# Performance work log

Hardware: AMD Instinct MI355X
Metric: run time of the kernel (lower is better)

## Reference

```python
import jax, jax.numpy as jnp
import numpy as np

NU = 100000  # num 'user' nodes
NI = 100000  # num 'item' nodes
E = 600000   # edges per relation
IN_DIM = 128
HID = 128
OUT = 64


def setup_inputs() -> dict:
    key = jax.random.key(0)
    ks = jax.random.split(key, 14)
    return {
        "x_user": jax.random.normal(ks[0], (NU, IN_DIM), jnp.float32),
        "x_item": jax.random.normal(ks[1], (NI, IN_DIM), jnp.float32),
        "W_proj": jax.random.normal(ks[2], (IN_DIM, HID), jnp.float32) / np.sqrt(IN_DIM),
        "b_proj": jax.random.normal(ks[3], (HID,), jnp.float32) * 0.01,
        "W_out": jax.random.normal(ks[4], (HID, OUT), jnp.float32) / np.sqrt(HID),
        "b_out": jax.random.normal(ks[5], (OUT,), jnp.float32) * 0.01,
        "al1": jax.random.normal(ks[6], (1,), jnp.float32),
        "ar1": jax.random.normal(ks[7], (1,), jnp.float32),
        "al2": jax.random.normal(ks[8], (1,), jnp.float32),
        "ar2": jax.random.normal(ks[9], (1,), jnp.float32),
        "e1_src": jax.random.randint(ks[10], (E,), 0, NU, jnp.int32),  # user->user
        "e1_dst": jax.random.randint(ks[11], (E,), 0, NU, jnp.int32),
        "e2_src": jax.random.randint(ks[12], (E,), 0, NI, jnp.int32),  # item->user
        "e2_dst": jax.random.randint(ks[13], (E,), 0, NU, jnp.int32),
    }


def reference(x_user, x_item, W_proj, b_proj, W_out, b_out,
              al1, ar1, al2, ar2, e1_src, e1_dst, e2_src, e2_dst):
    # Shared projection for every node type
    h_user = x_user @ W_proj + b_proj  # [NU, HID]
    h_item = x_item @ W_proj + b_proj  # [NI, HID]

    # Relation ('user','u2u','user'): msg = h_src*al + h_dst*ar, scatter-add to dst
    msg1 = h_user[e1_src] * al1 + h_user[e1_dst] * ar1  # [E, HID]
    out_user = jax.ops.segment_sum(msg1, e1_dst, num_segments=NU)

    # Relation ('item','i2u','user')
    msg2 = h_item[e2_src] * al2 + h_user[e2_dst] * ar2  # [E, HID]
    out_user = out_user + jax.ops.segment_sum(msg2, e2_dst, num_segments=NU)

    # 'item' receives no messages -> zeros
    out_item = jnp.zeros_like(h_item)

    out_user = jax.nn.elu(out_user)
    out_item = jax.nn.elu(out_item)

    # out_layer applied only to 'user'
    out_user = out_user @ W_out + b_out  # [NU, OUT]
    return out_user, out_item
```

## Files before the change

### kernel.cpp

```cpp
#include <hip/hip_runtime.h>
#include <hip/hip_bf16.h>
#include <math.h>

#define NUSER 100000
#define NITEM 100000
#define NEDGE 600000
#define HID   128
#define OUTD  64
#define LDA   136
#define LDF   132
#define PROJ_BLOCKS ((NUSER + NITEM) / 64)
#define EPB   ((2 * NEDGE + PROJ_BLOCKS - 1) / PROJ_BLOCKS)

typedef __attribute__((ext_vector_type(8))) short  bf16x8;
typedef __attribute__((ext_vector_type(4))) float  f32x4;
typedef __attribute__((ext_vector_type(4))) unsigned short u16x4;

__device__ inline unsigned short f2bf(float f) {
    __hip_bfloat16 h = __float2bfloat16(f);
    return *reinterpret_cast<unsigned short*>(&h);
}

__device__ inline void bf2x(unsigned int u, float& lo, float& hi) {
    union { unsigned int i; float f; } a, b;
    a.i = u << 16;
    b.i = u & 0xffff0000u;
    lo = a.f; hi = b.f;
}

__global__ void prep(const float* __restrict__ W, unsigned short* __restrict__ wt,
                     int* __restrict__ deg) {
    int i = blockIdx.x * 256 + threadIdx.x;
    if (i < 2 * NUSER) deg[i] = 0;
    if (i < 128 * 128) {
        int k = i >> 7, c = i & 127;
        wt[c * 128 + k] = f2bf(W[i]);
    }
}

__global__ void count_rank(const int* __restrict__ e1d, const int* __restrict__ e2d,
                           int* __restrict__ deg1, int* __restrict__ deg2,
                           int* __restrict__ rank) {
    int i = blockIdx.x * blockDim.x + threadIdx.x;
    if (i < NEDGE)            rank[i] = atomicAdd(&deg1[e1d[i]], 1);
    else if (i < 2 * NEDGE)   rank[i] = atomicAdd(&deg2[e2d[i - NEDGE]], 1);
}

#define SCAN_BLOCKS 391

__global__ __launch_bounds__(256) void scanA(
    const int* __restrict__ deg1, const int* __restrict__ deg2,
    int* __restrict__ off, int* __restrict__ bsum)
{
    __shared__ int sh[256];
    int t = threadIdx.x;
    int i = blockIdx.x * 256 + t;
    int d = (i < NUSER) ? deg1[i] + deg2[i] : 0;
    sh[t] = d;
    __syncthreads();
    for (int dd = 1; dd < 256; dd <<= 1) {
        int v = (t >= dd) ? sh[t - dd] : 0;
        __syncthreads();
        sh[t] += v;
        __syncthreads();
    }
    if (i < NUSER) off[i] = (t > 0) ? sh[t - 1] : 0;
    if (t == 255) bsum[blockIdx.x] = sh[255];
}

__global__ __launch_bounds__(512) void scanB(int* __restrict__ bsum, int* __restrict__ off) {
    __shared__ int sh[512];
    int t = threadIdx.x;
    int v = (t < SCAN_BLOCKS) ? bsum[t] : 0;
    sh[t] = v;
    __syncthreads();
    for (int dd = 1; dd < 512; dd <<= 1) {
        int x = (t >= dd) ? sh[t - dd] : 0;
        __syncthreads();
        sh[t] += x;
        __syncthreads();
    }
    if (t < SCAN_BLOCKS) bsum[t] = (t > 0) ? sh[t - 1] : 0;
    if (t == 511) off[NUSER] = sh[511];
}

__global__ __launch_bounds__(256) void scanC(int* __restrict__ off, const int* __restrict__ bsum) {
    int i = blockIdx.x * 256 + threadIdx.x;
    if (i < NUSER) off[i] += bsum[blockIdx.x];
}

__global__ __launch_bounds__(256) void proj_fill(
    const float* __restrict__ xu, const float* __restrict__ xi,
    const unsigned short* __restrict__ wt, const float* __restrict__ b,
    unsigned short* __restrict__ h,
    const int* __restrict__ e1s, const int* __restrict__ e1d,
    const int* __restrict__ e2s, const int* __restrict__ e2d,
    const int* __restrict__ off, const int* __restrict__ deg1,
    const int* __restrict__ rank, int* __restrict__ adj)
{
    __shared__ unsigned short Al[64 * LDA];
    const int tid = threadIdx.x;
    const int r0  = blockIdx.x * 64;

    float4 v[8];
    #pragma unroll
    for (int j = 0; j < 8; j++) {
        int i = tid + j * 256;
        int row = i >> 5, c4 = i & 31;
        int gr = r0 + row;
        const float4* src = (gr < NUSER)
            ? (const float4*)(xu + (size_t)gr * 128)
            : (const float4*)(xi + (size_t)(gr - NUSER) * 128);
        v[j] = src[c4];
    }
    #pragma unroll
    for (int j = 0; j < 8; j++) {
        int i = tid + j * 256;
        int row = i >> 5, c4 = i & 31;
        u16x4 p;
        p.x = f2bf(v[j].x); p.y = f2bf(v[j].y); p.z = f2bf(v[j].z); p.w = f2bf(v[j].w);
        *(u16x4*)&Al[row * LDA + c4 * 4] = p;
    }
    __syncthreads();

    const int w    = tid >> 6;
    const int lane = tid & 63;
    const int lrow = lane & 15;
    const int lk   = (lane >> 4) * 8;

    bf16x8 bfrag[4][2];
    #pragma unroll
    for (int kc = 0; kc < 4; kc++) {
        const int ko = kc * 32 + lk;
        bfrag[kc][0] = *(const bf16x8*)&wt[(size_t)(w * 32 + lrow) * 128 + ko];
        bfrag[kc][1] = *(const bf16x8*)&wt[(size_t)(w * 32 + 16 + lrow) * 128 + ko];
    }

    f32x4 acc[4][2] = {};
    #pragma unroll
    for (int kc = 0; kc < 4; kc++) {
        const int ko = kc * 32 + lk;
        #pragma unroll
        for (int rt = 0; rt < 4; rt++) {
            bf16x8 aa = *(const bf16x8*)&Al[(rt * 16 + lrow) * LDA + ko];
            acc[rt][0] = __builtin_amdgcn_mfma_f32_16x16x32_bf16(aa, bfrag[kc][0], acc[rt][0], 0, 0, 0);
            acc[rt][1] = __builtin_amdgcn_mfma_f32_16x16x32_bf16(aa, bfrag[kc][1], acc[rt][1], 0, 0, 0);
        }
    }

    __syncthreads();
    const float bv0 = b[w * 32 + lrow];
    const float bv1 = b[w * 32 + 16 + lrow];
    #pragma unroll
    for (int rt = 0; rt < 4; rt++) {
        #pragma unroll
        for (int ct = 0; ct < 2; ct++) {
            int col = w * 32 + ct * 16 + lrow;
            float bv = ct ? bv1 : bv0;
            #pragma unroll
            for (int r = 0; r < 4; r++) {
                int row = rt * 16 + (lane >> 4) * 4 + r;
                Al[row * LDA + col] = f2bf(acc[rt][ct][r] + bv);
            }
        }
    }
    __syncthreads();

    for (int i = tid; i < 1024; i += 256) {
        int row = i >> 4, c8 = i & 15;
        *(bf16x8*)&h[(size_t)(r0 + row) * 128 + c8 * 8] =
            *(const bf16x8*)&Al[row * LDA + c8 * 8];
    }

    const int base = blockIdx.x * EPB;
    const int lim  = (base + EPB < 2 * NEDGE) ? base + EPB : 2 * NEDGE;
    for (int i = base + tid; i < lim; i += 256) {
        int src, dst, slot;
        if (i < NEDGE) {
            src  = e1s[i];
            dst  = e1d[i];
            slot = off[dst] + rank[i];
        } else {
            int j = i - NEDGE;
            src  = NUSER + e2s[j];
            dst  = e2d[j];
            slot = off[dst] + deg1[dst] + rank[i];
        }
        adj[slot] = src;
    }
}

__global__ __launch_bounds__(256) void gather(
    const unsigned short* __restrict__ h, const int* __restrict__ adj,
    const int* __restrict__ off, const int* __restrict__ deg1,
    const int* __restrict__ deg2,
    const float* __restrict__ al1p, const float* __restrict__ ar1p,
    const float* __restrict__ al2p, const float* __restrict__ ar2p,
    unsigned int* __restrict__ accb)
{
    int wid  = (int)((blockIdx.x * 256 + threadIdx.x) >> 6);
    int lane = threadIdx.x & 63;
    if (wid >= NUSER) return;

    const unsigned int* h32 = (const unsigned int*)h;

    const float al1 = al1p[0], al2 = al2p[0];
    const float sc  = ar1p[0] * (float)deg1[wid] + ar2p[0] * (float)deg2[wid];

    float lo, hi;
    bf2x(h32[(size_t)wid * 64 + lane], lo, hi);
    float sx = sc * lo, sy = sc * hi;

    int e    = off[wid];
    int eend = off[wid + 1];

    for (; e + 8 <= eend; e += 8) {
        int s[8];
        #pragma unroll
        for (int j = 0; j < 8; j++) s[j] = adj[e + j];
        unsigned int u[8];
        #pragma unroll
        for (int j = 0; j < 8; j++) u[j] = h32[(size_t)s[j] * 64 + lane];
        #pragma unroll
        for (int j = 0; j < 8; j++) {
            float a = (s[j] < NUSER) ? al1 : al2;
            float x, y; bf2x(u[j], x, y);
            sx = fmaf(a, x, sx); sy = fmaf(a, y, sy);
        }
    }
    if (e + 4 <= eend) {
        int s[4];
        #pragma unroll
        for (int j = 0; j < 4; j++) s[j] = adj[e + j];
        unsigned int u[4];
        #pragma unroll
        for (int j = 0; j < 4; j++) u[j] = h32[(size_t)s[j] * 64 + lane];
        #pragma unroll
        for (int j = 0; j < 4; j++) {
            float a = (s[j] < NUSER) ? al1 : al2;
            float x, y; bf2x(u[j], x, y);
            sx = fmaf(a, x, sx); sy = fmaf(a, y, sy);
        }
        e += 4;
    }
    for (; e < eend; e++) {
        int s0 = adj[e];
        float a0 = (s0 < NUSER) ? al1 : al2;
        float x0, y0;
        bf2x(h32[(size_t)s0 * 64 + lane], x0, y0);
        sx = fmaf(a0, x0, sx); sy = fmaf(a0, y0, sy);
    }

    sx = sx > 0.f ? sx : expm1f(sx);
    sy = sy > 0.f ? sy : expm1f(sy);
    unsigned int pk = ((unsigned int)f2bf(sy) << 16) | (unsigned int)f2bf(sx);
    accb[(size_t)wid * 64 + lane] = pk;
}

__global__ __launch_bounds__(256) void finalize(
    const unsigned int* __restrict__ accb, const float* __restrict__ Wo,
    const float* __restrict__ bo, float* __restrict__ out)
{
    __shared__ float Wl[128 * 64];
    __shared__ float Al[64 * LDF];
    const int tid = threadIdx.x;
    const int n0  = blockIdx.x * 64;

    for (int i = tid; i < 128 * 64 / 4; i += 256)
        ((float4*)Wl)[i] = ((const float4*)Wo)[i];

    for (int i = tid; i < 4096; i += 256) {
        int row = i >> 6, d = i & 63;
        int gr = n0 + row;
        float lo = 0.f, hi = 0.f;
        if (gr < NUSER) bf2x(accb[(size_t)gr * 64 + d], lo, hi);
        *(float2*)&Al[row * LDF + d * 2] = make_float2(lo, hi);
    }
    __syncthreads();

    const int tr = tid >> 4;
    const int tc = tid & 15;

    float s[4][4];
    {
        float4 bv = *(const float4*)&bo[tc * 4];
        #pragma unroll
        for (int i = 0; i < 4; i++) {
            s[i][0] = bv.x; s[i][1] = bv.y; s[i][2] = bv.z; s[i][3] = bv.w;
        }
    }

    for (int k0 = 0; k0 < 128; k0 += 4) {
        float4 av[4];
        #pragma unroll
        for (int i = 0; i < 4; i++)
            av[i] = *(const float4*)&Al[(tr * 4 + i) * LDF + k0];
        #pragma unroll
        for (int kk = 0; kk < 4; kk++) {
            float4 wv = *(const float4*)&Wl[(k0 + kk) * 64 + tc * 4];
            #pragma unroll
            for (int i = 0; i < 4; i++) {
                float a = (&av[i].x)[kk];
                s[i][0] = fmaf(a, wv.x, s[i][0]);
                s[i][1] = fmaf(a, wv.y, s[i][1]);
                s[i][2] = fmaf(a, wv.z, s[i][2]);
                s[i][3] = fmaf(a, wv.w, s[i][3]);
            }
        }
    }

    #pragma unroll
    for (int i = 0; i < 4; i++) {
        int gr = n0 + tr * 4 + i;
        if (gr < NUSER) {
            float4 o = make_float4(s[i][0], s[i][1], s[i][2], s[i][3]);
            *(float4*)&out[(size_t)gr * 64 + tc * 4] = o;
        }
    }
}

extern "C" void kernel_launch(void* const* d_in, const int* in_sizes, int n_in,
                              void* d_out, int out_size, void* d_ws, size_t ws_size,
                              hipStream_t stream) {
    const float* xu  = (const float*)d_in[0];
    const float* xi  = (const float*)d_in[1];
    const float* Wp  = (const float*)d_in[2];
    const float* bp  = (const float*)d_in[3];
    const float* Wo  = (const float*)d_in[4];
    const float* bo  = (const float*)d_in[5];
    const float* al1 = (const float*)d_in[6];
    const float* ar1 = (const float*)d_in[7];
    const float* al2 = (const float*)d_in[8];
    const float* ar2 = (const float*)d_in[9];
    const int* e1s = (const int*)d_in[10];
    const int* e1d = (const int*)d_in[11];
    const int* e2s = (const int*)d_in[12];
    const int* e2d = (const int*)d_in[13];

    float* out   = (float*)d_out;
    float* oitem = out + (size_t)NUSER * OUTD;

    unsigned short* h    = (unsigned short*)d_ws;
    unsigned short* wt   = h + (size_t)(NUSER + NITEM) * HID;
    unsigned int*   accb = (unsigned int*)(wt + 128 * 128);

    int* meta = (int*)out;
    int* deg1 = meta;
    int* deg2 = meta + NUSER;
    int* off  = meta + 2 * NUSER;
    int* bsum = meta + 3 * NUSER + 64;
    int* adj  = meta + 3 * NUSER + 1024;
    int* rank = adj + 2 * NEDGE;

    hipMemsetAsync(oitem, 0, (size_t)NITEM * HID * sizeof(float), stream);

    prep<<<(2 * NUSER + 255) / 256, 256, 0, stream>>>(Wp, wt, deg1);

    count_rank<<<(2 * NEDGE + 255) / 256, 256, 0, stream>>>(e1d, e2d, deg1, deg2, rank);

    scanA<<<SCAN_BLOCKS, 256, 0, stream>>>(deg1, deg2, off, bsum);
    scanB<<<1, 512, 0, stream>>>(bsum, off);
    scanC<<<SCAN_BLOCKS, 256, 0, stream>>>(off, bsum);

    proj_fill<<<PROJ_BLOCKS, 256, 0, stream>>>(xu, xi, wt, bp, h,
                                               e1s, e1d, e2s, e2d,
                                               off, deg1, rank, adj);

    gather<<<(NUSER * 64) / 256, 256, 0, stream>>>(h, adj, off, deg1, deg2,
                                                   al1, ar1, al2, ar2, accb);

    finalize<<<(NUSER + 63) / 64, 256, 0, stream>>>(accb, Wo, bo, out);
}
```

Measured before the change: 227.4 us.

## Process two nodes per wave in gather and enlarge projection tiles

The gather kernel now gives each wavefront two destination nodes and interleaves their neighbor loads, so more independent memory requests are in flight per wave. The projection kernel moves from 64-row to 128-row tiles, staged in two halves, with a clamped item index, bounds-checked stores and a fixed three-iteration edge-fill loop. count_rank handles two edges per thread. Together these aim to hide gather latency and cut launch and block overhead, at the cost of higher register pressure, fewer waves in flight, and imbalance when the paired nodes have different degrees.

```diff
diff --git a/kernel.cpp b/kernel.cpp
--- a/kernel.cpp
+++ b/kernel.cpp
@@ -9,7 +9,8 @@
 #define OUTD  64
 #define LDA   136
 #define LDF   132
-#define PROJ_BLOCKS ((NUSER + NITEM) / 64)
+#define BLKR  128
+#define PROJ_BLOCKS ((NUSER + NITEM + BLKR - 1) / BLKR)
 #define EPB   ((2 * NEDGE + PROJ_BLOCKS - 1) / PROJ_BLOCKS)
 
 typedef __attribute__((ext_vector_type(8))) short  bf16x8;
@@ -38,12 +39,18 @@
     }
 }
 
+__device__ inline void cr_one(int i, const int* e1d, const int* e2d,
+                              int* deg1, int* deg2, int* rank) {
+    if (i < NEDGE)            rank[i] = atomicAdd(&deg1[e1d[i]], 1);
+    else if (i < 2 * NEDGE)   rank[i] = atomicAdd(&deg2[e2d[i - NEDGE]], 1);
+}
+
 __global__ void count_rank(const int* __restrict__ e1d, const int* __restrict__ e2d,
                            int* __restrict__ deg1, int* __restrict__ deg2,
                            int* __restrict__ rank) {
-    int i = blockIdx.x * blockDim.x + threadIdx.x;
-    if (i < NEDGE)            rank[i] = atomicAdd(&deg1[e1d[i]], 1);
-    else if (i < 2 * NEDGE)   rank[i] = atomicAdd(&deg2[e2d[i - NEDGE]], 1);
+    int i0 = blockIdx.x * 512 + threadIdx.x;
+    cr_one(i0, e1d, e2d, deg1, deg2, rank);
+    cr_one(i0 + 256, e1d, e2d, deg1, deg2, rank);
 }
 
 #define SCAN_BLOCKS 391
@@ -98,28 +105,36 @@
     const int* __restrict__ off, const int* __restrict__ deg1,
     const int* __restrict__ rank, int* __restrict__ adj)
 {
-    __shared__ unsigned short Al[64 * LDA];
+    __shared__ unsigned short Al[BLKR * LDA];
     const int tid = threadIdx.x;
-    const int r0  = blockIdx.x * 64;
-
-    float4 v[8];
-    #pragma unroll
-    for (int j = 0; j < 8; j++) {
-        int i = tid + j * 256;
-        int row = i >> 5, c4 = i & 31;
-        int gr = r0 + row;
-        const float4* src = (gr < NUSER)
-            ? (const float4*)(xu + (size_t)gr * 128)
-            : (const float4*)(xi + (size_t)(gr - NUSER) * 128);
-        v[j] = src[c4];
-    }
-    #pragma unroll
-    for (int j = 0; j < 8; j++) {
-        int i = tid + j * 256;
-        int row = i >> 5, c4 = i & 31;
-        u16x4 p;
-        p.x = f2bf(v[j].x); p.y = f2bf(v[j].y); p.z = f2bf(v[j].z); p.w = f2bf(v[j].w);
-        *(u16x4*)&Al[row * LDA + c4 * 4] = p;
+    const int r0  = blockIdx.x * BLKR;
+
+    #pragma unroll
+    for (int half = 0; half < 2; half++) {
+        float4 v[8];
+        #pragma unroll
+        for (int j = 0; j < 8; j++) {
+            int i = tid + (half * 8 + j) * 256;
+            int row = i >> 5, c4 = i & 31;
+            int gr = r0 + row;
+            const float* srcp;
+            if (gr < NUSER) srcp = xu + (size_t)gr * 128;
+            else {
+                int g2 = gr - NUSER;
+                if (g2 > NITEM - 1) g2 = NITEM - 1;
+                srcp = xi + (size_t)g2 * 128;
+            }
+            v[j] = ((const float4*)srcp)[c4];
+        }
+        __builtin_amdgcn_sched_barrier(0);
+        #pragma unroll
+        for (int j = 0; j < 8; j++) {
+            int i = tid + (half * 8 + j) * 256;
+            int row = i >> 5, c4 = i & 31;
+            u16x4 p;
+            p.x = f2bf(v[j].x); p.y = f2bf(v[j].y); p.z = f2bf(v[j].z); p.w = f2bf(v[j].w);
+            *(u16x4*)&Al[row * LDA + c4 * 4] = p;
+        }
     }
     __syncthreads();
 
@@ -136,12 +151,12 @@
         bfrag[kc][1] = *(const bf16x8*)&wt[(size_t)(w * 32 + 16 + lrow) * 128 + ko];
     }
 
-    f32x4 acc[4][2] = {};
+    f32x4 acc[8][2] = {};
     #pragma unroll
     for (int kc = 0; kc < 4; kc++) {
         const int ko = kc * 32 + lk;
         #pragma unroll
-        for (int rt = 0; rt < 4; rt++) {
+        for (int rt = 0; rt < 8; rt++) {
             bf16x8 aa = *(const bf16x8*)&Al[(rt * 16 + lrow) * LDA + ko];
             acc[rt][0] = __builtin_amdgcn_mfma_f32_16x16x32_bf16(aa, bfrag[kc][0], acc[rt][0], 0, 0, 0);
             acc[rt][1] = __builtin_amdgcn_mfma_f32_16x16x32_bf16(aa, bfrag[kc][1], acc[rt][1], 0, 0, 0);
@@ -152,7 +167,7 @@
     const float bv0 = b[w * 32 + lrow];
     const float bv1 = b[w * 32 + 16 + lrow];
     #pragma unroll
-    for (int rt = 0; rt < 4; rt++) {
+    for (int rt = 0; rt < 8; rt++) {
         #pragma unroll
         for (int ct = 0; ct < 2; ct++) {
             int col = w * 32 + ct * 16 + lrow;
@@ -166,15 +181,21 @@
     }
     __syncthreads();
 
-    for (int i = tid; i < 1024; i += 256) {
+    #pragma unroll
+    for (int j = 0; j < 8; j++) {
+        int i = tid + j * 256;
         int row = i >> 4, c8 = i & 15;
-        *(bf16x8*)&h[(size_t)(r0 + row) * 128 + c8 * 8] =
-            *(const bf16x8*)&Al[row * LDA + c8 * 8];
+        int gr = r0 + row;
+        if (gr < NUSER + NITEM)
+            *(bf16x8*)&h[(size_t)gr * 128 + c8 * 8] =
+                *(const bf16x8*)&Al[row * LDA + c8 * 8];
     }
 
     const int base = blockIdx.x * EPB;
-    const int lim  = (base + EPB < 2 * NEDGE) ? base + EPB : 2 * NEDGE;
-    for (int i = base + tid; i < lim; i += 256) {
+    #pragma unroll
+    for (int t = 0; t < 3; t++) {
+        int i = base + tid + t * 256;
+        if (i >= 2 * NEDGE) continue;
         int src, dst, slot;
         if (i < NEDGE) {
             src  = e1s[i];
@@ -198,40 +219,53 @@
     const float* __restrict__ al2p, const float* __restrict__ ar2p,
     unsigned int* __restrict__ accb)
 {
-    int wid  = (int)((blockIdx.x * 256 + threadIdx.x) >> 6);
+    int wv   = (int)((blockIdx.x * 256 + threadIdx.x) >> 6);
     int lane = threadIdx.x & 63;
-    if (wid >= NUSER) return;
+    if (wv >= NUSER / 2) return;
+    const int nA = 2 * wv, nB = 2 * wv + 1;
 
     const unsigned int* h32 = (const unsigned int*)h;
-
     const float al1 = al1p[0], al2 = al2p[0];
-    const float sc  = ar1p[0] * (float)deg1[wid] + ar2p[0] * (float)deg2[wid];
-
-    float lo, hi;
-    bf2x(h32[(size_t)wid * 64 + lane], lo, hi);
-    float sx = sc * lo, sy = sc * hi;
-
-    int e    = off[wid];
-    int eend = off[wid + 1];
-
-    for (; e + 8 <= eend; e += 8) {
-        int s[8];
-        #pragma unroll
-        for (int j = 0; j < 8; j++) s[j] = adj[e + j];
-        unsigned int u[8];
-        #pragma unroll
-        for (int j = 0; j < 8; j++) u[j] = h32[(size_t)s[j] * 64 + lane];
-        #pragma unroll
-        for (int j = 0; j < 8; j++) {
-            float a = (s[j] < NUSER) ? al1 : al2;
-            float x, y; bf2x(u[j], x, y);
-            sx = fmaf(a, x, sx); sy = fmaf(a, y, sy);
-        }
-    }
-    if (e + 4 <= eend) {
+    const float ar1 = ar1p[0], ar2 = ar2p[0];
+
+    int offA = off[nA], offM = off[nA + 1], offE = off[nA + 2];
+    const float scA = ar1 * (float)deg1[nA] + ar2 * (float)deg2[nA];
+    const float scB = ar1 * (float)deg1[nB] + ar2 * (float)deg2[nB];
+
+    float xA, yA, xB, yB;
+    bf2x(h32[(size_t)nA * 64 + lane], xA, yA);
+    bf2x(h32[(size_t)nB * 64 + lane], xB, yB);
+    float sxA = scA * xA, syA = scA * yA;
+    float sxB = scB * xB, syB = scB * yB;
+
+    int eA = offA, endA = offM;
+    int eB = offM, endB = offE;
+
+    while (eA + 4 <= endA && eB + 4 <= endB) {
+        int sA[4], sB[4];
+        #pragma unroll
+        for (int j = 0; j < 4; j++) { sA[j] = adj[eA + j]; sB[j] = adj[eB + j]; }
+        unsigned int uA[4], uB[4];
+        #pragma unroll
+        for (int j = 0; j < 4; j++) {
+            uA[j] = h32[(size_t)sA[j] * 64 + lane];
+            uB[j] = h32[(size_t)sB[j] * 64 + lane];
+        }
+        #pragma unroll
+        for (int j = 0; j < 4; j++) {
+            float a = (sA[j] < NUSER) ? al1 : al2;
+            float x, y; bf2x(uA[j], x, y);
+            sxA = fmaf(a, x, sxA); syA = fmaf(a, y, syA);
+            float b2 = (sB[j] < NUSER) ? al1 : al2;
+            bf2x(uB[j], x, y);
+            sxB = fmaf(b2, x, sxB); syB = fmaf(b2, y, syB);
+        }
+        eA += 4; eB += 4;
+    }
+    while (eA + 4 <= endA) {
         int s[4];
         #pragma unroll
-        for (int j = 0; j < 4; j++) s[j] = adj[e + j];
+        for (int j = 0; j < 4; j++) s[j] = adj[eA + j];
         unsigned int u[4];
         #pragma unroll
         for (int j = 0; j < 4; j++) u[j] = h32[(size_t)s[j] * 64 + lane];
@@ -239,22 +273,44 @@
         for (int j = 0; j < 4; j++) {
             float a = (s[j] < NUSER) ? al1 : al2;
             float x, y; bf2x(u[j], x, y);
-            sx = fmaf(a, x, sx); sy = fmaf(a, y, sy);
-        }
-        e += 4;
-    }
-    for (; e < eend; e++) {
-        int s0 = adj[e];
-        float a0 = (s0 < NUSER) ? al1 : al2;
-        float x0, y0;
-        bf2x(h32[(size_t)s0 * 64 + lane], x0, y0);
-        sx = fmaf(a0, x0, sx); sy = fmaf(a0, y0, sy);
-    }
-
-    sx = sx > 0.f ? sx : expm1f(sx);
-    sy = sy > 0.f ? sy : expm1f(sy);
-    unsigned int pk = ((unsigned int)f2bf(sy) << 16) | (unsigned int)f2bf(sx);
-    accb[(size_t)wid * 64 + lane] = pk;
+            sxA = fmaf(a, x, sxA); syA = fmaf(a, y, syA);
+        }
+        eA += 4;
+    }
+    for (; eA < endA; eA++) {
+        int s0 = adj[eA];
+        float a = (s0 < NUSER) ? al1 : al2;
+        float x, y; bf2x(h32[(size_t)s0 * 64 + lane], x, y);
+        sxA = fmaf(a, x, sxA); syA = fmaf(a, y, syA);
+    }
+    while (eB + 4 <= endB) {
+        int s[4];
+        #pragma unroll
+        for (int j = 0; j < 4; j++) s[j] = adj[eB + j];
+        unsigned int u[4];
+        #pragma unroll
+        for (int j = 0; j < 4; j++) u[j] = h32[(size_t)s[j] * 64 + lane];
+        #pragma unroll
+        for (int j = 0; j < 4; j++) {
+            float a = (s[j] < NUSER) ? al1 : al2;
+            float x, y; bf2x(u[j], x, y);
+            sxB = fmaf(a, x, sxB); syB = fmaf(a, y, syB);
+        }
+        eB += 4;
+    }
+    for (; eB < endB; eB++) {
+        int s0 = adj[eB];
+        float a = (s0 < NUSER) ? al1 : al2;
+        float x, y; bf2x(h32[(size_t)s0 * 64 + lane], x, y);
+        sxB = fmaf(a, x, sxB); syB = fmaf(a, y, syB);
+    }
+
+    sxA = sxA > 0.f ? sxA : expm1f(sxA);
+    syA = syA > 0.f ? syA : expm1f(syA);
+    sxB = sxB > 0.f ? sxB : expm1f(sxB);
+    syB = syB > 0.f ? syB : expm1f(syB);
+    accb[(size_t)nA * 64 + lane] = ((unsigned int)f2bf(syA) << 16) | (unsigned int)f2bf(sxA);
+    accb[(size_t)nB * 64 + lane] = ((unsigned int)f2bf(syB) << 16) | (unsigned int)f2bf(sxB);
 }
 
 __global__ __launch_bounds__(256) void finalize(
@@ -356,7 +412,7 @@
 
     prep<<<(2 * NUSER + 255) / 256, 256, 0, stream>>>(Wp, wt, deg1);
 
-    count_rank<<<(2 * NEDGE + 255) / 256, 256, 0, stream>>>(e1d, e2d, deg1, deg2, rank);
+    count_rank<<<(2 * NEDGE + 511) / 512, 256, 0, stream>>>(e1d, e2d, deg1, deg2, rank);
 
     scanA<<<SCAN_BLOCKS, 256, 0, stream>>>(deg1, deg2, off, bsum);
     scanB<<<1, 512, 0, stream>>>(bsum, off);
@@ -366,8 +422,8 @@
                                                e1s, e1d, e2s, e2d,
                                                off, deg1, rank, adj);
 
-    gather<<<(NUSER * 64) / 256, 256, 0, stream>>>(h, adj, off, deg1, deg2,
-                                                   al1, ar1, al2, ar2, accb);
+    gather<<<(NUSER / 2 * 64) / 256, 256, 0, stream>>>(h, adj, off, deg1, deg2,
+                                                       al1, ar1, al2, ar2, accb);
 
     finalize<<<(NUSER + 63) / 64, 256, 0, stream>>>(accb, Wo, bo, out);
 }
```

New measurement: 232.0 us. 1.02x slower.
